# Kernel optimization log

Hardware: AMD Instinct MI355X
Metric: run time of the kernel (lower is better)

The kernel has to match this reference:

```python
import jax, jax.numpy as jnp
import numpy as np

N_NODES = 50000
N_EDGES = 800000
DIMS = [128, 256, 256]
EPS = 1e-5


def setup_inputs() -> dict:
    key = jax.random.key(0)
    ks = jax.random.split(key, 8)
    x = jax.random.normal(ks[0], (N_NODES, DIMS[0]), dtype=jnp.float32)
    edge_index = jax.random.randint(ks[1], (2, N_EDGES), 0, N_NODES, dtype=jnp.int64)
    inp = {"x": x, "edge_index": edge_index}
    for i in range(2):
        din, dout = DIMS[i], DIMS[i + 1]
        # Glorot init for GCN weight; zeros bias; BN gamma=1, beta=0; PReLU a=0.25
        scale = jnp.sqrt(2.0 / (din + dout)).astype(jnp.float32)
        inp[f"W{i}"] = jax.random.normal(ks[2 + i], (din, dout), dtype=jnp.float32) * scale
        inp[f"b{i}"] = jnp.zeros((dout,), dtype=jnp.float32)
        inp[f"gamma{i}"] = jnp.ones((dout,), dtype=jnp.float32)
        inp[f"beta{i}"] = jnp.zeros((dout,), dtype=jnp.float32)
        inp[f"a{i}"] = jnp.full((1,), 0.25, dtype=jnp.float32)
    return inp


def _gcn_bn_prelu(x, src, dst, w_edge, W, b, gamma, beta, a):
    n = x.shape[0]
    h = x @ W  # [N, dout]
    # symmetric GCN normalization with self-loops already appended to src/dst
    deg = jax.ops.segment_sum(w_edge, dst, num_segments=n)  # [N]
    dinv = jnp.where(deg > 0, jax.lax.rsqrt(deg), 0.0)
    norm = dinv[src] * w_edge * dinv[dst]  # [E+N]
    msgs = h[src] * norm[:, None]  # [E+N, dout] gather + scale
    out = jax.ops.segment_sum(msgs, dst, num_segments=n) + b
    # BatchNorm1d (training-mode batch statistics, biased variance)
    mean = jnp.mean(out, axis=0)
    var = jnp.mean(jnp.square(out - mean), axis=0)
    y = (out - mean) * jax.lax.rsqrt(var + EPS) * gamma + beta
    # PReLU with a single shared parameter
    return jnp.where(y > 0, y, a[0] * y)


def reference(x, edge_index, W0, b0, gamma0, beta0, a0, W1, b1, gamma1, beta1, a1):
    n = x.shape[0]
    loops = jnp.arange(n, dtype=edge_index.dtype)
    src = jnp.concatenate([edge_index[0], loops])
    dst = jnp.concatenate([edge_index[1], loops])
    w_edge = jnp.ones(src.shape[0], dtype=x.dtype)
    h = _gcn_bn_prelu(x, src, dst, w_edge, W0, b0, gamma0, beta0, a0)
    h = _gcn_bn_prelu(h, src, dst, w_edge, W1, b1, gamma1, beta1, a1)
    return h
```

## Files before the change

kernel.cpp:

```cpp
#include <hip/hip_runtime.h>

typedef unsigned int u32;
typedef unsigned short u16;
typedef unsigned long long u64;

using f32x4 = __attribute__((ext_vector_type(4))) float;
using bf16x8 = __attribute__((ext_vector_type(8))) short;

#define BN_EPS 1e-5f

__device__ __forceinline__ float bflo(u32 u) {
    union { u32 u; float f; } v; v.u = u << 16; return v.f;
}
__device__ __forceinline__ float bfhi(u32 u) {
    union { u32 u; float f; } v; v.u = u & 0xffff0000u; return v.f;
}
__device__ __forceinline__ u32 f2bf(float f) {
    union { float f; u32 u; } v; v.f = f;
    return (v.u + 0x7fffu + ((v.u >> 16) & 1u)) >> 16;
}

__global__ void detect_k(const void* ei, int* flag, int nnode) {
    const u64* p = (const u64*)ei;
    int lane = threadIdx.x & 63;
    u64 v = p[lane];
    int ok = (v < (u64)nnode);
    int all64 = __all(ok);
    if (threadIdx.x == 0) *flag = all64 ? 1 : 0;
}

__global__ void deg_count_k(const void* ei, const int* __restrict__ flag,
                            int* __restrict__ degi, int E) {
    int is64 = *flag;
    int i = blockIdx.x * blockDim.x + threadIdx.x;
    int stride = gridDim.x * blockDim.x;
    if (is64) {
        const long long* p = (const long long*)ei;
        for (; i < E; i += stride) atomicAdd(&degi[(int)p[(size_t)E + i]], 1);
    } else {
        const int* p = (const int*)ei;
        for (; i < E; i += stride) atomicAdd(&degi[p[(size_t)E + i]], 1);
    }
}

__global__ void dinv_k(const int* __restrict__ degi, float* __restrict__ dinv, int n) {
    int i = blockIdx.x * blockDim.x + threadIdx.x;
    int stride = gridDim.x * blockDim.x;
    for (; i < n; i += stride) dinv[i] = rsqrtf((float)(degi[i] + 1));
}

__global__ void block_sum_k(const int* __restrict__ counts, int* __restrict__ bsum, int n) {
    __shared__ int red[4];
    int idx = blockIdx.x * 256 + threadIdx.x;
    int v = (idx < n) ? counts[idx] : 0;
#pragma unroll
    for (int m = 32; m >= 1; m >>= 1) v += __shfl_xor(v, m);
    int lane = threadIdx.x & 63, w = threadIdx.x >> 6;
    if (lane == 0) red[w] = v;
    __syncthreads();
    if (threadIdx.x == 0) bsum[blockIdx.x] = red[0] + red[1] + red[2] + red[3];
}

__global__ void scan_bsum_k(int* bsum, int nb) {
    __shared__ int sd[256];
    int t = threadIdx.x;
    int v = (t < nb) ? bsum[t] : 0;
    sd[t] = v; __syncthreads();
    for (int off = 1; off < 256; off <<= 1) {
        int u = (t >= off) ? sd[t - off] : 0;
        __syncthreads();
        sd[t] += u;
        __syncthreads();
    }
    if (t < nb) bsum[t] = sd[t] - v;
}

__global__ void block_scan_k(const int* __restrict__ counts, const int* __restrict__ bsum,
                             int* __restrict__ rp, int n) {
    __shared__ int sd[256];
    int t = threadIdx.x;
    int idx = blockIdx.x * 256 + t;
    int v = (idx < n) ? counts[idx] : 0;
    sd[t] = v; __syncthreads();
    for (int off = 1; off < 256; off <<= 1) {
        int u = (t >= off) ? sd[t - off] : 0;
        __syncthreads();
        sd[t] += u;
        __syncthreads();
    }
    if (idx < n) rp[idx + 1] = bsum[blockIdx.x] + sd[t];
    if (blockIdx.x == 0 && t == 0) rp[0] = 0;
}

__global__ void csr_fill_k(const void* ei, const int* __restrict__ flag,
                           const float* __restrict__ dinv, const int* __restrict__ rp,
                           int* __restrict__ fill, uint2* __restrict__ csrv, int E) {
    int is64 = *flag;
    int i = blockIdx.x * blockDim.x + threadIdx.x;
    int stride = gridDim.x * blockDim.x;
    for (; i < E; i += stride) {
        int s, d;
        if (is64) {
            const long long* p = (const long long*)ei;
            s = (int)p[i]; d = (int)p[(size_t)E + i];
        } else {
            const int* p = (const int*)ei;
            s = p[i]; d = p[(size_t)E + i];
        }
        int pos = atomicAdd(&fill[d], 1);
        csrv[rp[d] + pos] = make_uint2((u32)s, __float_as_uint(dinv[s]));
    }
}

__global__ void f32_to_bf16_k(const float* __restrict__ in, u16* __restrict__ out, int nquads) {
    int i = blockIdx.x * blockDim.x + threadIdx.x;
    int stride = gridDim.x * blockDim.x;
    for (; i < nquads; i += stride) {
        float4 v = ((const float4*)in)[i];
        u32 lo = f2bf(v.x) | (f2bf(v.y) << 16);
        u32 hi = f2bf(v.z) | (f2bf(v.w) << 16);
        ((uint2*)out)[i] = make_uint2(lo, hi);
    }
}

__global__ void transpose_w_k(const float* __restrict__ W, u16* __restrict__ Wt,
                              int din, int dout) {
    int i = blockIdx.x * blockDim.x + threadIdx.x;
    int total = din * dout;
    if (i < total) {
        int r = i / dout, c = i % dout;
        Wt[(size_t)c * din + r] = (u16)f2bf(W[i]);
    }
}

template <int DIN>
__global__ __launch_bounds__(256) void aggregate_k(
    const u16* __restrict__ H, u16* __restrict__ O,
    const float* __restrict__ dinv, const int* __restrict__ rp,
    const uint2* __restrict__ csrv, int n)
{
    constexpr int RL = DIN / 8;
    constexpr int EPW = 64 / RL;
    int node = blockIdx.x * 4 + (threadIdx.x >> 6);
    if (node >= n) return;
    int lane = threadIdx.x & 63;
    int li = lane & (RL - 1);
    int g = lane / RL;

    float acc[8];
    float dv = dinv[node];
    if (g == 0) {
        uint4 r = *(const uint4*)(H + (size_t)node * DIN + li * 8);
        acc[0] = dv * bflo(r.x); acc[1] = dv * bfhi(r.x);
        acc[2] = dv * bflo(r.y); acc[3] = dv * bfhi(r.y);
        acc[4] = dv * bflo(r.z); acc[5] = dv * bfhi(r.z);
        acc[6] = dv * bflo(r.w); acc[7] = dv * bfhi(r.w);
    } else {
#pragma unroll
        for (int j = 0; j < 8; ++j) acc[j] = 0.f;
    }

    int e0 = rp[node], e1 = rp[node + 1];
    for (int e = e0 + g; e < e1; e += EPW) {
        uint2 cv = csrv[e];
        uint4 r = *(const uint4*)(H + (size_t)cv.x * DIN + li * 8);
        float w = __uint_as_float(cv.y);
        acc[0] = fmaf(w, bflo(r.x), acc[0]);
        acc[1] = fmaf(w, bfhi(r.x), acc[1]);
        acc[2] = fmaf(w, bflo(r.y), acc[2]);
        acc[3] = fmaf(w, bfhi(r.y), acc[3]);
        acc[4] = fmaf(w, bflo(r.z), acc[4]);
        acc[5] = fmaf(w, bfhi(r.z), acc[5]);
        acc[6] = fmaf(w, bflo(r.w), acc[6]);
        acc[7] = fmaf(w, bfhi(r.w), acc[7]);
    }

#pragma unroll
    for (int j = 0; j < 8; ++j) {
        if (EPW == 4) acc[j] += __shfl_xor(acc[j], 16);
        acc[j] += __shfl_xor(acc[j], 32);
    }

    if (g == 0) {
        uint4 o;
        o.x = f2bf(acc[0] * dv) | (f2bf(acc[1] * dv) << 16);
        o.y = f2bf(acc[2] * dv) | (f2bf(acc[3] * dv) << 16);
        o.z = f2bf(acc[4] * dv) | (f2bf(acc[5] * dv) << 16);
        o.w = f2bf(acc[6] * dv) | (f2bf(acc[7] * dv) << 16);
        *(uint4*)(O + (size_t)node * DIN + li * 8) = o;
    }
}

template <int K, int OUTB>
__global__ __launch_bounds__(256) void gemm_bf16(
    const u16* __restrict__ A, const u16* __restrict__ Bt,
    const float* __restrict__ bias, void* __restrict__ outp,
    float* __restrict__ part, int M)
{
    __shared__ __align__(16) u16 lA[4096];
    __shared__ __align__(16) u16 lB[4096];
    __shared__ float red[256];
    const int tid = threadIdx.x;
    const int lane = tid & 63;
    const int wid = tid >> 6;
    const int wm = wid >> 1, wn = wid & 1;
    const int l15 = lane & 15, khi = lane >> 4;
    const int row0 = blockIdx.x * 128;
    const int col0 = blockIdx.y * 128;

    f32x4 acc[4][4];
#pragma unroll
    for (int i = 0; i < 4; ++i)
#pragma unroll
        for (int j = 0; j < 4; ++j)
            acc[i][j] = (f32x4){0.f, 0.f, 0.f, 0.f};

    if (tid < 256) red[tid] = 0.f;

    for (int k0 = 0; k0 < K; k0 += 32) {
#pragma unroll
        for (int t = 0; t < 2; ++t) {
            int c = t * 256 + wid * 64 + lane;
            int r = c & 127, kh = c >> 7;
            int ar = row0 + r; if (ar > M - 1) ar = M - 1;
            const u16* ga = A + (size_t)ar * K + k0 + kh * 8;
            u16* la = &lA[(t * 256 + wid * 64) * 8];
            __builtin_amdgcn_global_load_lds(
                (const __attribute__((address_space(1))) void*)ga,
                (__attribute__((address_space(3))) void*)la, 16, 0, 0);
            const u16* gb = Bt + (size_t)(col0 + r) * K + k0 + kh * 8;
            u16* lb = &lB[(t * 256 + wid * 64) * 8];
            __builtin_amdgcn_global_load_lds(
                (const __attribute__((address_space(1))) void*)gb,
                (__attribute__((address_space(3))) void*)lb, 16, 0, 0);
        }
        __syncthreads();
        bf16x8 afr[4], bfr[4];
#pragma unroll
        for (int mi = 0; mi < 4; ++mi)
            afr[mi] = *(const bf16x8*)&lA[khi * 1024 + (wm * 64 + mi * 16 + l15) * 8];
#pragma unroll
        for (int nj = 0; nj < 4; ++nj)
            bfr[nj] = *(const bf16x8*)&lB[khi * 1024 + (wn * 64 + nj * 16 + l15) * 8];
#pragma unroll
        for (int mi = 0; mi < 4; ++mi)
#pragma unroll
            for (int nj = 0; nj < 4; ++nj)
                acc[mi][nj] = __builtin_amdgcn_mfma_f32_16x16x32_bf16(
                    afr[mi], bfr[nj], acc[mi][nj], 0, 0, 0);
        __syncthreads();
    }

#pragma unroll
    for (int mi = 0; mi < 4; ++mi) {
#pragma unroll
        for (int nj = 0; nj < 4; ++nj) {
            int coll = wn * 64 + nj * 16 + l15;
            int colg = col0 + coll;
            float bsv = bias[colg];
            float s = 0.f, q = 0.f;
#pragma unroll
            for (int i = 0; i < 4; ++i) {
                int rowg = row0 + wm * 64 + mi * 16 + khi * 4 + i;
                if (rowg < M) {
                    float v = acc[mi][nj][i] + bsv;
                    if (OUTB) ((u16*)outp)[(size_t)rowg * 256 + colg] = (u16)f2bf(v);
                    else      ((float*)outp)[(size_t)rowg * 256 + colg] = v;
                    s += v; q += v * v;
                }
            }
            s += __shfl_xor(s, 16); s += __shfl_xor(s, 32);
            q += __shfl_xor(q, 16); q += __shfl_xor(q, 32);
            if (lane < 16) {
                atomicAdd(&red[coll * 2], s);
                atomicAdd(&red[coll * 2 + 1], q);
            }
        }
    }
    __syncthreads();
    if (tid < 256)
        part[(size_t)blockIdx.x * 512 + blockIdx.y * 256 + tid] = red[tid];
}

__global__ __launch_bounds__(256) void bn_stats_k(
    const float* __restrict__ part, const float* __restrict__ gamma,
    const float* __restrict__ beta, float* __restrict__ ss, int nbx, int M)
{
    int wave = threadIdx.x >> 6;
    int lane = threadIdx.x & 63;
    int c = blockIdx.x * 4 + wave;
    int base = (c >> 7) * 256 + (c & 127) * 2;
    float s = 0.f, q = 0.f;
    for (int bx = lane; bx < nbx; bx += 64) {
        float2 v = *(const float2*)&part[(size_t)bx * 512 + base];
        s += v.x; q += v.y;
    }
#pragma unroll
    for (int m = 32; m >= 1; m >>= 1) {
        s += __shfl_xor(s, m);
        q += __shfl_xor(q, m);
    }
    if (lane == 0) {
        float mean = s / (float)M;
        float var = fmaxf(q / (float)M - mean * mean, 0.f);
        float sc = gamma[c] * rsqrtf(var + BN_EPS);
        ss[c] = sc;
        ss[256 + c] = beta[c] - mean * sc;
    }
}

template <int INB, int OUTB>
__global__ void bn_prelu_k(const void* __restrict__ in, void* __restrict__ outp,
                           const float* __restrict__ ss,
                           const float* __restrict__ aptr, int nquads) {
    float a = aptr[0];
    int i = blockIdx.x * blockDim.x + threadIdx.x;
    int stride = gridDim.x * blockDim.x;
    for (; i < nquads; i += stride) {
        float v0, v1, v2, v3;
        if (INB) {
            uint2 u = ((const uint2*)in)[i];
            v0 = bflo(u.x); v1 = bfhi(u.x); v2 = bflo(u.y); v3 = bfhi(u.y);
        } else {
            float4 v = ((const float4*)in)[i];
            v0 = v.x; v1 = v.y; v2 = v.z; v3 = v.w;
        }
        int c0 = (i * 4) & 255;
        float r0 = v0 * ss[c0 + 0] + ss[256 + c0 + 0];
        float r1 = v1 * ss[c0 + 1] + ss[256 + c0 + 1];
        float r2 = v2 * ss[c0 + 2] + ss[256 + c0 + 2];
        float r3 = v3 * ss[c0 + 3] + ss[256 + c0 + 3];
        r0 = r0 > 0.f ? r0 : a * r0;
        r1 = r1 > 0.f ? r1 : a * r1;
        r2 = r2 > 0.f ? r2 : a * r2;
        r3 = r3 > 0.f ? r3 : a * r3;
        if (OUTB) {
            u32 lo = f2bf(r0) | (f2bf(r1) << 16);
            u32 hi = f2bf(r2) | (f2bf(r3) << 16);
            ((uint2*)outp)[i] = make_uint2(lo, hi);
        } else {
            ((float4*)outp)[i] = make_float4(r0, r1, r2, r3);
        }
    }
}

extern "C" void kernel_launch(void* const* d_in, const int* in_sizes, int n_in,
                              void* d_out, int out_size, void* d_ws, size_t ws_size,
                              hipStream_t stream) {
    const float* x   = (const float*)d_in[0];
    const void*  ei  = d_in[1];
    const float* W0  = (const float*)d_in[2];
    const float* b0  = (const float*)d_in[3];
    const float* g0  = (const float*)d_in[4];
    const float* be0 = (const float*)d_in[5];
    const float* a0  = (const float*)d_in[6];
    const float* W1  = (const float*)d_in[7];
    const float* b1  = (const float*)d_in[8];
    const float* g1  = (const float*)d_in[9];
    const float* be1 = (const float*)d_in[10];
    const float* a1  = (const float*)d_in[11];
    float* out = (float*)d_out;

    const int n = in_sizes[0] / 128;
    const int E = in_sizes[1] / 2;
    const int nbx = (n + 127) / 128;

    char* ws = (char*)d_ws;
    size_t off = 0;
    auto alloc = [&](size_t bytes) {
        size_t r = off; off += (bytes + 255) & ~(size_t)255; return r;
    };
    size_t o_deg  = alloc((size_t)n * 4);
    size_t o_fill = alloc((size_t)n * 4);
    size_t o_rp   = alloc((size_t)(n + 1) * 4);
    size_t o_bsum = alloc(4096);
    size_t o_flag = alloc(256);
    size_t o_dinv = alloc((size_t)n * 4);
    size_t o_csr  = alloc((size_t)E * 8);
    size_t o_part = alloc((size_t)nbx * 512 * 4);
    size_t o_ss   = alloc(2048);
    size_t o_wt0  = alloc(256 * 128 * 2);
    size_t o_wt1  = alloc(256 * 256 * 2);
    size_t o_xh   = alloc((size_t)n * 128 * 2);
    size_t o_agg0 = alloc((size_t)n * 128 * 2);
    size_t o_y0   = alloc((size_t)n * 256 * 2);
    size_t o_agg1 = o_xh;

    int*   degi  = (int*)(ws + o_deg);
    int*   fill  = (int*)(ws + o_fill);
    int*   rp    = (int*)(ws + o_rp);
    int*   bsum  = (int*)(ws + o_bsum);
    int*   flag  = (int*)(ws + o_flag);
    float* dinv  = (float*)(ws + o_dinv);
    uint2* csrv  = (uint2*)(ws + o_csr);
    float* part  = (float*)(ws + o_part);
    float* ssbuf = (float*)(ws + o_ss);
    u16*   wt0   = (u16*)(ws + o_wt0);
    u16*   wt1   = (u16*)(ws + o_wt1);
    u16*   xh    = (u16*)(ws + o_xh);
    u16*   agg0  = (u16*)(ws + o_agg0);
    u16*   y0    = (u16*)(ws + o_y0);
    u16*   agg1  = (u16*)(ws + o_agg1);

    hipMemsetAsync(ws + o_deg, 0, (size_t)n * 4, stream);
    hipMemsetAsync(ws + o_fill, 0, (size_t)n * 4, stream);

    const int gE = (E + 255) / 256 < 4096 ? (E + 255) / 256 : 4096;
    const int gN = (n + 255) / 256;

    detect_k<<<1, 64, 0, stream>>>(ei, flag, n);
    deg_count_k<<<gE, 256, 0, stream>>>(ei, flag, degi, E);
    dinv_k<<<gN, 256, 0, stream>>>(degi, dinv, n);
    block_sum_k<<<gN, 256, 0, stream>>>(degi, bsum, n);
    scan_bsum_k<<<1, 256, 0, stream>>>(bsum, gN);
    block_scan_k<<<gN, 256, 0, stream>>>(degi, bsum, rp, n);
    csr_fill_k<<<gE, 256, 0, stream>>>(ei, flag, dinv, rp, fill, csrv, E);

    f32_to_bf16_k<<<4096, 256, 0, stream>>>(x, xh, n * 128 / 4);
    transpose_w_k<<<(128 * 256 + 255) / 256, 256, 0, stream>>>(W0, wt0, 128, 256);
    transpose_w_k<<<(256 * 256 + 255) / 256, 256, 0, stream>>>(W1, wt1, 256, 256);

    const dim3 ggrid(nbx, 2);

    aggregate_k<128><<<(n + 3) / 4, 256, 0, stream>>>(xh, agg0, dinv, rp, csrv, n);
    gemm_bf16<128, 1><<<ggrid, 256, 0, stream>>>(agg0, wt0, b0, d_out, part, n);
    bn_stats_k<<<64, 256, 0, stream>>>(part, g0, be0, ssbuf, nbx, n);
    bn_prelu_k<1, 1><<<4096, 256, 0, stream>>>(d_out, y0, ssbuf, a0, n * 256 / 4);

    aggregate_k<256><<<(n + 3) / 4, 256, 0, stream>>>(y0, agg1, dinv, rp, csrv, n);
    gemm_bf16<256, 1><<<ggrid, 256, 0, stream>>>(agg1, wt1, b1, y0, part, n);
    bn_stats_k<<<64, 256, 0, stream>>>(part, g1, be1, ssbuf, nbx, n);
    bn_prelu_k<1, 0><<<4096, 256, 0, stream>>>(y0, out, ssbuf, a1, n * 256 / 4);
}
```

Baseline: 319.2 us.

## Store node features in 32-column slices for cache-local sparse aggregation

Node feature matrices now use a sliced layout, with 32-column slices stored contiguously for all nodes. Aggregation blocks each process one slice, so every gathered neighbour row is 64 bytes within a smaller working set that fits the cache better. The CSR now stores only source indices, and the edge weight is read from dinv inside the gather, which halves CSR memory. In exchange the CSR is walked once per slice, and the GEMM A-loads plus the BN/PReLU writes are adapted to the sliced layout.

New measurement: 357.7 us. +12.0%, slower.

```diff
diff --git a/kernel.cpp b/kernel.cpp
--- a/kernel.cpp
+++ b/kernel.cpp
@@ -93,8 +93,8 @@
 }
 
 __global__ void csr_fill_k(const void* ei, const int* __restrict__ flag,
-                           const float* __restrict__ dinv, const int* __restrict__ rp,
-                           int* __restrict__ fill, uint2* __restrict__ csrv, int E) {
+                           const int* __restrict__ rp, int* __restrict__ fill,
+                           int* __restrict__ csr, int E) {
     int is64 = *flag;
     int i = blockIdx.x * blockDim.x + threadIdx.x;
     int stride = gridDim.x * blockDim.x;
@@ -108,18 +108,22 @@
             s = p[i]; d = p[(size_t)E + i];
         }
         int pos = atomicAdd(&fill[d], 1);
-        csrv[rp[d] + pos] = make_uint2((u32)s, __float_as_uint(dinv[s]));
-    }
-}
-
-__global__ void f32_to_bf16_k(const float* __restrict__ in, u16* __restrict__ out, int nquads) {
-    int i = blockIdx.x * blockDim.x + threadIdx.x;
-    int stride = gridDim.x * blockDim.x;
-    for (; i < nquads; i += stride) {
+        csr[rp[d] + pos] = s;
+    }
+}
+
+__global__ void f32_to_bf16_sm_k(const float* __restrict__ in, u16* __restrict__ out, int n) {
+    int i = blockIdx.x * blockDim.x + threadIdx.x;
+    int stride = gridDim.x * blockDim.x;
+    int total = n * 32;
+    for (; i < total; i += stride) {
+        int row = i >> 5;
+        int c0 = (i & 31) * 4;
         float4 v = ((const float4*)in)[i];
         u32 lo = f2bf(v.x) | (f2bf(v.y) << 16);
         u32 hi = f2bf(v.z) | (f2bf(v.w) << 16);
-        ((uint2*)out)[i] = make_uint2(lo, hi);
+        int slice = c0 >> 5, off = c0 & 31;
+        *(uint2*)(out + (size_t)slice * n * 32 + (size_t)row * 32 + off) = make_uint2(lo, hi);
     }
 }
 
@@ -137,65 +141,50 @@
 __global__ __launch_bounds__(256) void aggregate_k(
     const u16* __restrict__ H, u16* __restrict__ O,
     const float* __restrict__ dinv, const int* __restrict__ rp,
-    const uint2* __restrict__ csrv, int n)
+    const int* __restrict__ csr, int n)
 {
-    constexpr int RL = DIN / 8;
-    constexpr int EPW = 64 / RL;
-    int node = blockIdx.x * 4 + (threadIdx.x >> 6);
+    constexpr int NS = DIN / 32;
+    int b = blockIdx.x;
+    int slice = b % NS;
+    int lane = threadIdx.x & 63;
+    int g = lane >> 2, li = lane & 3;
+    int node = (b / NS) * 64 + (threadIdx.x >> 6) * 16 + g;
     if (node >= n) return;
-    int lane = threadIdx.x & 63;
-    int li = lane & (RL - 1);
-    int g = lane / RL;
-
+    const u16* Hs = H + (size_t)slice * n * 32;
+    float dv = dinv[node];
+    uint4 r = *(const uint4*)(Hs + (size_t)node * 32 + li * 8);
     float acc[8];
-    float dv = dinv[node];
-    if (g == 0) {
-        uint4 r = *(const uint4*)(H + (size_t)node * DIN + li * 8);
-        acc[0] = dv * bflo(r.x); acc[1] = dv * bfhi(r.x);
-        acc[2] = dv * bflo(r.y); acc[3] = dv * bfhi(r.y);
-        acc[4] = dv * bflo(r.z); acc[5] = dv * bfhi(r.z);
-        acc[6] = dv * bflo(r.w); acc[7] = dv * bfhi(r.w);
-    } else {
-#pragma unroll
-        for (int j = 0; j < 8; ++j) acc[j] = 0.f;
-    }
-
-    int e0 = rp[node], e1 = rp[node + 1];
-    for (int e = e0 + g; e < e1; e += EPW) {
-        uint2 cv = csrv[e];
-        uint4 r = *(const uint4*)(H + (size_t)cv.x * DIN + li * 8);
-        float w = __uint_as_float(cv.y);
-        acc[0] = fmaf(w, bflo(r.x), acc[0]);
-        acc[1] = fmaf(w, bfhi(r.x), acc[1]);
-        acc[2] = fmaf(w, bflo(r.y), acc[2]);
-        acc[3] = fmaf(w, bfhi(r.y), acc[3]);
-        acc[4] = fmaf(w, bflo(r.z), acc[4]);
-        acc[5] = fmaf(w, bfhi(r.z), acc[5]);
-        acc[6] = fmaf(w, bflo(r.w), acc[6]);
-        acc[7] = fmaf(w, bfhi(r.w), acc[7]);
-    }
-
-#pragma unroll
-    for (int j = 0; j < 8; ++j) {
-        if (EPW == 4) acc[j] += __shfl_xor(acc[j], 16);
-        acc[j] += __shfl_xor(acc[j], 32);
-    }
-
-    if (g == 0) {
-        uint4 o;
-        o.x = f2bf(acc[0] * dv) | (f2bf(acc[1] * dv) << 16);
-        o.y = f2bf(acc[2] * dv) | (f2bf(acc[3] * dv) << 16);
-        o.z = f2bf(acc[4] * dv) | (f2bf(acc[5] * dv) << 16);
-        o.w = f2bf(acc[6] * dv) | (f2bf(acc[7] * dv) << 16);
-        *(uint4*)(O + (size_t)node * DIN + li * 8) = o;
-    }
+    acc[0] = dv * bflo(r.x); acc[1] = dv * bfhi(r.x);
+    acc[2] = dv * bflo(r.y); acc[3] = dv * bfhi(r.y);
+    acc[4] = dv * bflo(r.z); acc[5] = dv * bfhi(r.z);
+    acc[6] = dv * bflo(r.w); acc[7] = dv * bfhi(r.w);
+    int e1 = rp[node + 1];
+    for (int e = rp[node]; e < e1; ++e) {
+        int s = csr[e];
+        float wgt = dinv[s];
+        uint4 rr = *(const uint4*)(Hs + (size_t)s * 32 + li * 8);
+        acc[0] = fmaf(wgt, bflo(rr.x), acc[0]);
+        acc[1] = fmaf(wgt, bfhi(rr.x), acc[1]);
+        acc[2] = fmaf(wgt, bflo(rr.y), acc[2]);
+        acc[3] = fmaf(wgt, bfhi(rr.y), acc[3]);
+        acc[4] = fmaf(wgt, bflo(rr.z), acc[4]);
+        acc[5] = fmaf(wgt, bfhi(rr.z), acc[5]);
+        acc[6] = fmaf(wgt, bflo(rr.w), acc[6]);
+        acc[7] = fmaf(wgt, bfhi(rr.w), acc[7]);
+    }
+    uint4 o;
+    o.x = f2bf(acc[0] * dv) | (f2bf(acc[1] * dv) << 16);
+    o.y = f2bf(acc[2] * dv) | (f2bf(acc[3] * dv) << 16);
+    o.z = f2bf(acc[4] * dv) | (f2bf(acc[5] * dv) << 16);
+    o.w = f2bf(acc[6] * dv) | (f2bf(acc[7] * dv) << 16);
+    *(uint4*)(O + (size_t)slice * n * 32 + (size_t)node * 32 + li * 8) = o;
 }
 
 template <int K, int OUTB>
 __global__ __launch_bounds__(256) void gemm_bf16(
     const u16* __restrict__ A, const u16* __restrict__ Bt,
     const float* __restrict__ bias, void* __restrict__ outp,
-    float* __restrict__ part, int M)
+    float* __restrict__ part, int M, int An)
 {
     __shared__ __align__(16) u16 lA[4096];
     __shared__ __align__(16) u16 lB[4096];
@@ -218,12 +207,13 @@
     if (tid < 256) red[tid] = 0.f;
 
     for (int k0 = 0; k0 < K; k0 += 32) {
+        const u16* Asl = A + (size_t)(k0 >> 5) * An * 32;
 #pragma unroll
         for (int t = 0; t < 2; ++t) {
             int c = t * 256 + wid * 64 + lane;
             int r = c & 127, kh = c >> 7;
             int ar = row0 + r; if (ar > M - 1) ar = M - 1;
-            const u16* ga = A + (size_t)ar * K + k0 + kh * 8;
+            const u16* ga = Asl + (size_t)ar * 32 + kh * 8;
             u16* la = &lA[(t * 256 + wid * 64) * 8];
             __builtin_amdgcn_global_load_lds(
                 (const __attribute__((address_space(1))) void*)ga,
@@ -306,6 +296,41 @@
         float sc = gamma[c] * rsqrtf(var + BN_EPS);
         ss[c] = sc;
         ss[256 + c] = beta[c] - mean * sc;
+    }
+}
+
+__global__ void bn_prelu_sm_k(const u16* __restrict__ in, u16* __restrict__ out,
+                              const float* __restrict__ ss, const float* __restrict__ aptr,
+                              int n) {
+    float a = aptr[0];
+    int i = blockIdx.x * blockDim.x + threadIdx.x;
+    int stride = gridDim.x * blockDim.x;
+    int total = n * 32;
+    for (; i < total; i += stride) {
+        int row = i >> 5;
+        int c0 = (i & 31) * 8;
+        uint4 u = *(const uint4*)(in + (size_t)row * 256 + c0);
+        float f0 = bflo(u.x), f1 = bfhi(u.x), f2 = bflo(u.y), f3 = bfhi(u.y);
+        float f4 = bflo(u.z), f5 = bfhi(u.z), f6 = bflo(u.w), f7 = bfhi(u.w);
+        float r0 = f0 * ss[c0 + 0] + ss[256 + c0 + 0];
+        float r1 = f1 * ss[c0 + 1] + ss[256 + c0 + 1];
+        float r2 = f2 * ss[c0 + 2] + ss[256 + c0 + 2];
+        float r3 = f3 * ss[c0 + 3] + ss[256 + c0 + 3];
+        float r4 = f4 * ss[c0 + 4] + ss[256 + c0 + 4];
+        float r5 = f5 * ss[c0 + 5] + ss[256 + c0 + 5];
+        float r6 = f6 * ss[c0 + 6] + ss[256 + c0 + 6];
+        float r7 = f7 * ss[c0 + 7] + ss[256 + c0 + 7];
+        r0 = r0 > 0.f ? r0 : a * r0;  r1 = r1 > 0.f ? r1 : a * r1;
+        r2 = r2 > 0.f ? r2 : a * r2;  r3 = r3 > 0.f ? r3 : a * r3;
+        r4 = r4 > 0.f ? r4 : a * r4;  r5 = r5 > 0.f ? r5 : a * r5;
+        r6 = r6 > 0.f ? r6 : a * r6;  r7 = r7 > 0.f ? r7 : a * r7;
+        uint4 o;
+        o.x = f2bf(r0) | (f2bf(r1) << 16);
+        o.y = f2bf(r2) | (f2bf(r3) << 16);
+        o.z = f2bf(r4) | (f2bf(r5) << 16);
+        o.w = f2bf(r6) | (f2bf(r7) << 16);
+        int slice = c0 >> 5, off = c0 & 31;
+        *(uint4*)(out + (size_t)slice * n * 32 + (size_t)row * 32 + off) = o;
     }
 }
 
@@ -376,7 +401,7 @@
     size_t o_bsum = alloc(4096);
     size_t o_flag = alloc(256);
     size_t o_dinv = alloc((size_t)n * 4);
-    size_t o_csr  = alloc((size_t)E * 8);
+    size_t o_csr  = alloc((size_t)E * 4);
     size_t o_part = alloc((size_t)nbx * 512 * 4);
     size_t o_ss   = alloc(2048);
     size_t o_wt0  = alloc(256 * 128 * 2);
@@ -384,7 +409,8 @@
     size_t o_xh   = alloc((size_t)n * 128 * 2);
     size_t o_agg0 = alloc((size_t)n * 128 * 2);
     size_t o_y0   = alloc((size_t)n * 256 * 2);
-    size_t o_agg1 = o_xh;
+    size_t o_agg1 = alloc((size_t)n * 256 * 2);
+    size_t o_z1   = o_xh;
 
     int*   degi  = (int*)(ws + o_deg);
     int*   fill  = (int*)(ws + o_fill);
@@ -392,7 +418,7 @@
     int*   bsum  = (int*)(ws + o_bsum);
     int*   flag  = (int*)(ws + o_flag);
     float* dinv  = (float*)(ws + o_dinv);
-    uint2* csrv  = (uint2*)(ws + o_csr);
+    int*   csr   = (int*)(ws + o_csr);
     float* part  = (float*)(ws + o_part);
     float* ssbuf = (float*)(ws + o_ss);
     u16*   wt0   = (u16*)(ws + o_wt0);
@@ -401,12 +427,14 @@
     u16*   agg0  = (u16*)(ws + o_agg0);
     u16*   y0    = (u16*)(ws + o_y0);
     u16*   agg1  = (u16*)(ws + o_agg1);
+    u16*   z1    = (u16*)(ws + o_z1);
 
     hipMemsetAsync(ws + o_deg, 0, (size_t)n * 4, stream);
     hipMemsetAsync(ws + o_fill, 0, (size_t)n * 4, stream);
 
     const int gE = (E + 255) / 256 < 4096 ? (E + 255) / 256 : 4096;
     const int gN = (n + 255) / 256;
+    const int chunks = (n + 63) / 64;
 
     detect_k<<<1, 64, 0, stream>>>(ei, flag, n);
     deg_count_k<<<gE, 256, 0, stream>>>(ei, flag, degi, E);
@@ -414,21 +442,21 @@
     block_sum_k<<<gN, 256, 0, stream>>>(degi, bsum, n);
     scan_bsum_k<<<1, 256, 0, stream>>>(bsum, gN);
     block_scan_k<<<gN, 256, 0, stream>>>(degi, bsum, rp, n);
-    csr_fill_k<<<gE, 256, 0, stream>>>(ei, flag, dinv, rp, fill, csrv, E);
-
-    f32_to_bf16_k<<<4096, 256, 0, stream>>>(x, xh, n * 128 / 4);
+    csr_fill_k<<<gE, 256, 0, stream>>>(ei, flag, rp, fill, csr, E);
+
+    f32_to_bf16_sm_k<<<4096, 256, 0, stream>>>(x, xh, n);
     transpose_w_k<<<(128 * 256 + 255) / 256, 256, 0, stream>>>(W0, wt0, 128, 256);
     transpose_w_k<<<(256 * 256 + 255) / 256, 256, 0, stream>>>(W1, wt1, 256, 256);
 
     const dim3 ggrid(nbx, 2);
 
-    aggregate_k<128><<<(n + 3) / 4, 256, 0, stream>>>(xh, agg0, dinv, rp, csrv, n);
-    gemm_bf16<128, 1><<<ggrid, 256, 0, stream>>>(agg0, wt0, b0, d_out, part, n);
+    aggregate_k<128><<<4 * chunks, 256, 0, stream>>>(xh, agg0, dinv, rp, csr, n);
+    gemm_bf16<128, 1><<<ggrid, 256, 0, stream>>>(agg0, wt0, b0, d_out, part, n, n);
     bn_stats_k<<<64, 256, 0, stream>>>(part, g0, be0, ssbuf, nbx, n);
-    bn_prelu_k<1, 1><<<4096, 256, 0, stream>>>(d_out, y0, ssbuf, a0, n * 256 / 4);
-
-    aggregate_k<256><<<(n + 3) / 4, 256, 0, stream>>>(y0, agg1, dinv, rp, csrv, n);
-    gemm_bf16<256, 1><<<ggrid, 256, 0, stream>>>(agg1, wt1, b1, y0, part, n);
+    bn_prelu_sm_k<<<4096, 256, 0, stream>>>((const u16*)d_out, y0, ssbuf, a0, n);
+
+    aggregate_k<256><<<8 * chunks, 256, 0, stream>>>(y0, agg1, dinv, rp, csr, n);
+    gemm_bf16<256, 1><<<ggrid, 256, 0, stream>>>(agg1, wt1, b1, z1, part, n, n);
     bn_stats_k<<<64, 256, 0, stream>>>(part, g1, be1, ssbuf, nbx, n);
-    bn_prelu_k<1, 0><<<4096, 256, 0, stream>>>(y0, out, ssbuf, a1, n * 256 / 4);
-}
+    bn_prelu_k<1, 0><<<4096, 256, 0, stream>>>(z1, out, ssbuf, a1, n * 256 / 4);
+}
```
